# Kernel tuning notes

Measured on AMD Instinct MI355X. Metric: run time of the kernel, lower is better.

## Reference

```python
import jax, jax.numpy as jnp
import numpy as np

TEMPERATURE = 0.1
N, D = 4096, 1024


def setup_inputs() -> dict:
    key = jax.random.key(0)
    k1, k2 = jax.random.split(key)
    return {
        "embeddings1": jax.random.normal(k1, (N, D), dtype=jnp.float32),
        "embeddings2": jax.random.normal(k2, (N, D), dtype=jnp.float32),
    }


def reference(embeddings1, embeddings2):
    # L2-normalize rows (eps matches torch F.normalize default 1e-12)
    e1 = embeddings1 / jnp.maximum(jnp.linalg.norm(embeddings1, axis=1, keepdims=True), 1e-12)
    e2 = embeddings2 / jnp.maximum(jnp.linalg.norm(embeddings2, axis=1, keepdims=True), 1e-12)

    # [N, N] pairwise logits; one GEMM replaces the N^2 Python-loop dots
    logits = jnp.einsum("nd,md->nm", e1, e2) / TEMPERATURE
    expS = jnp.exp(logits)
    diag = jnp.diagonal(expS)

    # denominators EXCLUDE the diagonal term (as in the original loop slicing)
    row_denom = jnp.sum(expS, axis=1) - diag  # sum over j != i of exp(s_ij)
    col_denom = jnp.sum(expS, axis=0) - diag  # sum over i != j of exp(s_ij)

    log_diag = jnp.diagonal(logits)
    sim_12 = jnp.sum(log_diag - jnp.log(row_denom))
    sim_21 = jnp.sum(log_diag - jnp.log(col_denom))
    return (-sim_12, -sim_21)
```

## Files before the change

### kernel.cpp

```cpp
#include <hip/hip_runtime.h>
#include <hip/hip_bf16.h>
#include <stdint.h>

#define NN 4096
#define DD 1024
#define SCL (10.0f / 4096.0f)

typedef float f32x4 __attribute__((ext_vector_type(4)));
typedef long long i64;

__device__ __forceinline__ void gload_lds16(const void* g, void* l) {
  __builtin_amdgcn_global_load_lds(
      (const __attribute__((address_space(1))) void*)g,
      (__attribute__((address_space(3))) void*)l, 16, 0, 0);
}

__global__ __launch_bounds__(256) void nrm_kernel(
    const float* __restrict__ e1, const float* __restrict__ e2,
    uint32_t* __restrict__ e1q, uint32_t* __restrict__ e2q,
    float* __restrict__ log_diag, float* __restrict__ exp_diag,
    float* __restrict__ row_sum, float* __restrict__ col_sum)
{
  const int row  = blockIdx.x;
  const int tid  = threadIdx.x;
  const int lane = tid & 63;
  const int wave = tid >> 6;
  const int64_t base = (int64_t)row * DD;

  const float4 v1 = *reinterpret_cast<const float4*>(e1 + base + tid * 4);
  const float4 v2 = *reinterpret_cast<const float4*>(e2 + base + tid * 4);

  float ss1 = v1.x*v1.x + v1.y*v1.y + v1.z*v1.z + v1.w*v1.w;
  float ss2 = v2.x*v2.x + v2.y*v2.y + v2.z*v2.z + v2.w*v2.w;
  float d12 = v1.x*v2.x + v1.y*v2.y + v1.z*v2.z + v1.w*v2.w;

  #pragma unroll
  for (int off = 1; off < 64; off <<= 1) {
    ss1 += __shfl_xor(ss1, off);
    ss2 += __shfl_xor(ss2, off);
    d12 += __shfl_xor(d12, off);
  }

  __shared__ float red[3][4];
  if (lane == 0) { red[0][wave] = ss1; red[1][wave] = ss2; red[2][wave] = d12; }
  __syncthreads();
  ss1 = red[0][0] + red[0][1] + red[0][2] + red[0][3];
  ss2 = red[1][0] + red[1][1] + red[1][2] + red[1][3];
  d12 = red[2][0] + red[2][1] + red[2][2] + red[2][3];

  const float inv1 = 1.0f / fmaxf(sqrtf(ss1), 1e-12f);
  const float inv2 = 1.0f / fmaxf(sqrtf(ss2), 1e-12f);

  if (tid == 0) {
    const float ld = d12 * inv1 * inv2 * 10.0f;
    log_diag[row] = ld;
    exp_diag[row] = __expf(ld);
    row_sum[row] = 0.0f;
    col_sum[row] = 0.0f;
  }

  const float s1 = inv1 * 64.0f;
  const float s2 = inv2 * 64.0f;
  int u1 = __builtin_amdgcn_cvt_pk_fp8_f32(v1.x * s1, v1.y * s1, 0, false);
  u1     = __builtin_amdgcn_cvt_pk_fp8_f32(v1.z * s1, v1.w * s1, u1, true);
  int u2 = __builtin_amdgcn_cvt_pk_fp8_f32(v2.x * s2, v2.y * s2, 0, false);
  u2     = __builtin_amdgcn_cvt_pk_fp8_f32(v2.z * s2, v2.w * s2, u2, true);
  e1q[row * (DD / 4) + tid] = (uint32_t)u1;
  e2q[row * (DD / 4) + tid] = (uint32_t)u2;
}

__global__ __launch_bounds__(512, 4) void gemm_kernel(
    const uint8_t* __restrict__ A,
    const uint8_t* __restrict__ B,
    float* __restrict__ row_sum, float* __restrict__ col_sum)
{
  __shared__ __align__(16) uint8_t lds_a[2][256][64];
  __shared__ __align__(16) uint8_t lds_b[2][128][64];

  const int tid  = threadIdx.x;
  const int lane = tid & 63;
  const int wave = tid >> 6;
  const int wm = wave >> 1;
  const int wn = wave & 1;

  const int bid = blockIdx.x;
  const int xcd = bid & 7;
  const int k   = bid >> 3;
  const int brow = ((xcd >> 1) * 4 + (k >> 4)) * 256;
  const int bcol = ((xcd & 1) * 16 + (k & 15)) * 128;

  const int fr = lane & 15;
  const int fq = lane >> 4;
  const int y  = ((fr >> 1) & 3) << 1;
  const int o0 = ((fq ^ y) * 8);

  const int s_chunk = ((lane & 3) ^ ((lane >> 3) & 3)) * 16;
  const uint8_t* a_src0 = A + (int64_t)(brow + wave * 32 + (lane >> 2)) * DD + s_chunk;
  const uint8_t* a_src1 = a_src0 + 16 * DD;
  const uint8_t* b_src  = B + (int64_t)(bcol + wave * 16 + (lane >> 2)) * DD + s_chunk;

  f32x4 acc[4][4] = {};

#define STAGE(n, kc)                                          \
  gload_lds16(a_src0 + (kc), &lds_a[n][wave * 32][0]);        \
  gload_lds16(a_src1 + (kc), &lds_a[n][wave * 32 + 16][0]);   \
  gload_lds16(b_src  + (kc), &lds_b[n][wave * 16][0]);

#define TILE(c, PF, KC)                                                        \
  {                                                                            \
    asm volatile("s_waitcnt vmcnt(0)" ::: "memory");                           \
    __builtin_amdgcn_s_barrier();                                              \
    i64 a0[4], b0[4], a1[4], b1[4];                                            \
    _Pragma("unroll")                                                          \
    for (int i = 0; i < 4; ++i)                                                \
      a0[i] = *reinterpret_cast<const i64*>(&lds_a[c][wm*64 + i*16 + fr][o0]); \
    _Pragma("unroll")                                                          \
    for (int j = 0; j < 4; ++j)                                                \
      b0[j] = *reinterpret_cast<const i64*>(&lds_b[c][wn*64 + j*16 + fr][o0]); \
    _Pragma("unroll")                                                          \
    for (int i = 0; i < 4; ++i)                                                \
      a1[i] = *reinterpret_cast<const i64*>(                                   \
          &lds_a[c][wm*64 + i*16 + fr][o0 ^ 32]);                              \
    _Pragma("unroll")                                                          \
    for (int j = 0; j < 4; ++j)                                                \
      b1[j] = *reinterpret_cast<const i64*>(                                   \
          &lds_b[c][wn*64 + j*16 + fr][o0 ^ 32]);                              \
    if (PF) { STAGE((c) ^ 1, KC) }                                             \
    __builtin_amdgcn_s_setprio(1);                                             \
    _Pragma("unroll")                                                          \
    for (int i = 0; i < 4; ++i) {                                              \
      _Pragma("unroll")                                                        \
      for (int j = 0; j < 4; ++j)                                              \
        acc[i][j] = __builtin_amdgcn_mfma_f32_16x16x32_fp8_fp8(                \
            a0[i], b0[j], acc[i][j], 0, 0, 0);                                 \
    }                                                                          \
    _Pragma("unroll")                                                          \
    for (int i = 0; i < 4; ++i) {                                              \
      _Pragma("unroll")                                                        \
      for (int j = 0; j < 4; ++j)                                              \
        acc[i][j] = __builtin_amdgcn_mfma_f32_16x16x32_fp8_fp8(                \
            a1[i], b1[j], acc[i][j], 0, 0, 0);                                 \
    }                                                                          \
    __builtin_amdgcn_s_setprio(0);                                             \
  }

  STAGE(0, 0)

  #pragma unroll 2
  for (int t = 0; t < DD / 64; ++t) {
    TILE(t & 1, t < DD / 64 - 1, (t + 1) * 64)
  }
#undef TILE
#undef STAGE

  float rowp[4][4];
  float colp[4];
  #pragma unroll
  for (int mi = 0; mi < 4; ++mi)
    #pragma unroll
    for (int j = 0; j < 4; ++j) rowp[mi][j] = 0.0f;
  #pragma unroll
  for (int ni = 0; ni < 4; ++ni) colp[ni] = 0.0f;

  #pragma unroll
  for (int mi = 0; mi < 4; ++mi) {
    #pragma unroll
    for (int ni = 0; ni < 4; ++ni) {
      #pragma unroll
      for (int j = 0; j < 4; ++j) {
        const float v = __expf(acc[mi][ni][j] * SCL);
        rowp[mi][j] += v;
        colp[ni]    += v;
      }
    }
  }

  #pragma unroll
  for (int mi = 0; mi < 4; ++mi) {
    #pragma unroll
    for (int j = 0; j < 4; ++j) {
      float r = rowp[mi][j];
      r += __shfl_xor(r, 1);
      r += __shfl_xor(r, 2);
      r += __shfl_xor(r, 4);
      r += __shfl_xor(r, 8);
      if (fr == 0) {
        atomicAdd(&row_sum[brow + wm * 64 + mi * 16 + fq * 4 + j], r);
      }
    }
  }
  #pragma unroll
  for (int ni = 0; ni < 4; ++ni) {
    float cc = colp[ni];
    cc += __shfl_xor(cc, 16);
    cc += __shfl_xor(cc, 32);
    if (lane < 16) {
      atomicAdd(&col_sum[bcol + wn * 64 + ni * 16 + fr], cc);
    }
  }
}

__global__ __launch_bounds__(1024) void fin_kernel(
    const float* __restrict__ row_sum, const float* __restrict__ col_sum,
    const float* __restrict__ log_diag, const float* __restrict__ exp_diag,
    float* __restrict__ out)
{
  const int tid  = threadIdx.x;
  const int lane = tid & 63;
  const int wave = tid >> 6;
  const float* sums = (blockIdx.x == 0) ? row_sum : col_sum;
  float a = 0.0f;
  #pragma unroll
  for (int kk = 0; kk < NN / 1024; ++kk) {
    const int i = tid + kk * 1024;
    a += logf(sums[i] - exp_diag[i]) - log_diag[i];
  }
  #pragma unroll
  for (int off = 1; off < 64; off <<= 1) a += __shfl_xor(a, off);
  __shared__ float r0[16];
  if (lane == 0) r0[wave] = a;
  __syncthreads();
  if (tid == 0) {
    float s = 0.0f;
    #pragma unroll
    for (int w = 0; w < 16; ++w) s += r0[w];
    out[blockIdx.x] = s;
  }
}

extern "C" void kernel_launch(void* const* d_in, const int* in_sizes, int n_in,
                              void* d_out, int out_size, void* d_ws, size_t ws_size,
                              hipStream_t stream) {
  const float* e1 = (const float*)d_in[0];
  const float* e2 = (const float*)d_in[1];
  float* out = (float*)d_out;

  char* ws = (char*)d_ws;
  uint32_t* e1q = (uint32_t*)ws;
  uint32_t* e2q = (uint32_t*)(ws + (size_t)NN * DD);
  float* log_diag = (float*)(ws + (size_t)NN * DD * 2);
  float* exp_diag = log_diag + NN;
  float* row_sum  = exp_diag + NN;
  float* col_sum  = row_sum + NN;

  nrm_kernel<<<NN, 256, 0, stream>>>(e1, e2, e1q, e2q, log_diag, exp_diag,
                                     row_sum, col_sum);
  gemm_kernel<<<512, 512, 0, stream>>>((const uint8_t*)e1q, (const uint8_t*)e2q,
                                       row_sum, col_sum);
  fin_kernel<<<2, 1024, 0, stream>>>(row_sum, col_sum, log_diag, exp_diag, out);
}
```

Measured before the change: 50.05 us.

## Enlarge GEMM block tile to 256x256 with triple-buffered LDS pipeline

The fp8 GEMM block tile grows from 256x128 to 256x256, so each wave now computes 128x64 outputs and the grid shrinks to 256 blocks. The LDS staging moves from a double buffer to a triple buffer with a prefetch distance of two and a partial vmcnt wait. Global-to-LDS loads are split into four pieces and interleaved between MFMA groups. The aim is better operand reuse and more overlap of memory loads with MFMA work. In exchange it uses more accumulator registers and more LDS, cuts occupancy to one block per CU, and leaves fewer blocks to spread the work.

```diff
diff --git a/kernel.cpp b/kernel.cpp
--- a/kernel.cpp
+++ b/kernel.cpp
@@ -69,101 +69,137 @@
   e2q[row * (DD / 4) + tid] = (uint32_t)u2;
 }
 
-__global__ __launch_bounds__(512, 4) void gemm_kernel(
+__global__ __launch_bounds__(512, 2) void gemm_kernel(
     const uint8_t* __restrict__ A,
     const uint8_t* __restrict__ B,
     float* __restrict__ row_sum, float* __restrict__ col_sum)
 {
-  __shared__ __align__(16) uint8_t lds_a[2][256][64];
-  __shared__ __align__(16) uint8_t lds_b[2][128][64];
+  __shared__ __align__(16) uint8_t lds_a[3][256][64];
+  __shared__ __align__(16) uint8_t lds_b[3][256][64];
 
   const int tid  = threadIdx.x;
   const int lane = tid & 63;
   const int wave = tid >> 6;
-  const int wm = wave >> 1;
-  const int wn = wave & 1;
+  const int wm = wave >> 2;
+  const int wn = wave & 3;
 
   const int bid = blockIdx.x;
   const int xcd = bid & 7;
   const int k   = bid >> 3;
-  const int brow = ((xcd >> 1) * 4 + (k >> 4)) * 256;
-  const int bcol = ((xcd & 1) * 16 + (k & 15)) * 128;
-
-  const int fr = lane & 15;
-  const int fq = lane >> 4;
-  const int y  = ((fr >> 1) & 3) << 1;
-  const int o0 = ((fq ^ y) * 8);
+  const int brow = ((xcd >> 1) * 4 + (k >> 3)) * 256;
+  const int bcol = ((xcd & 1) * 8 + (k & 7)) * 256;
+
+  const int fr  = lane & 15;
+  const int fq  = lane >> 4;
+  const int fq1 = fq & 1;
+  const int fq2 = fq >> 1;
+  const int frx = (fr >> 1) & 3;
+  const int o0  = ((fq2 ^ frx) << 4) + (fq1 << 3);
+  const int o1  = o0 ^ 32;
 
   const int s_chunk = ((lane & 3) ^ ((lane >> 3) & 3)) * 16;
-  const uint8_t* a_src0 = A + (int64_t)(brow + wave * 32 + (lane >> 2)) * DD + s_chunk;
-  const uint8_t* a_src1 = a_src0 + 16 * DD;
-  const uint8_t* b_src  = B + (int64_t)(bcol + wave * 16 + (lane >> 2)) * DD + s_chunk;
-
-  f32x4 acc[4][4] = {};
-
-#define STAGE(n, kc)                                          \
-  gload_lds16(a_src0 + (kc), &lds_a[n][wave * 32][0]);        \
-  gload_lds16(a_src1 + (kc), &lds_a[n][wave * 32 + 16][0]);   \
-  gload_lds16(b_src  + (kc), &lds_b[n][wave * 16][0]);
-
-#define TILE(c, PF, KC)                                                        \
-  {                                                                            \
-    asm volatile("s_waitcnt vmcnt(0)" ::: "memory");                           \
-    __builtin_amdgcn_s_barrier();                                              \
-    i64 a0[4], b0[4], a1[4], b1[4];                                            \
-    _Pragma("unroll")                                                          \
-    for (int i = 0; i < 4; ++i)                                                \
-      a0[i] = *reinterpret_cast<const i64*>(&lds_a[c][wm*64 + i*16 + fr][o0]); \
-    _Pragma("unroll")                                                          \
-    for (int j = 0; j < 4; ++j)                                                \
-      b0[j] = *reinterpret_cast<const i64*>(&lds_b[c][wn*64 + j*16 + fr][o0]); \
-    _Pragma("unroll")                                                          \
-    for (int i = 0; i < 4; ++i)                                                \
-      a1[i] = *reinterpret_cast<const i64*>(                                   \
-          &lds_a[c][wm*64 + i*16 + fr][o0 ^ 32]);                              \
-    _Pragma("unroll")                                                          \
-    for (int j = 0; j < 4; ++j)                                                \
-      b1[j] = *reinterpret_cast<const i64*>(                                   \
-          &lds_b[c][wn*64 + j*16 + fr][o0 ^ 32]);                              \
-    if (PF) { STAGE((c) ^ 1, KC) }                                             \
-    __builtin_amdgcn_s_setprio(1);                                             \
-    _Pragma("unroll")                                                          \
-    for (int i = 0; i < 4; ++i) {                                              \
-      _Pragma("unroll")                                                        \
-      for (int j = 0; j < 4; ++j)                                              \
-        acc[i][j] = __builtin_amdgcn_mfma_f32_16x16x32_fp8_fp8(                \
-            a0[i], b0[j], acc[i][j], 0, 0, 0);                                 \
-    }                                                                          \
-    _Pragma("unroll")                                                          \
-    for (int i = 0; i < 4; ++i) {                                              \
-      _Pragma("unroll")                                                        \
-      for (int j = 0; j < 4; ++j)                                              \
-        acc[i][j] = __builtin_amdgcn_mfma_f32_16x16x32_fp8_fp8(                \
-            a1[i], b1[j], acc[i][j], 0, 0, 0);                                 \
-    }                                                                          \
-    __builtin_amdgcn_s_setprio(0);                                             \
-  }
-
-  STAGE(0, 0)
-
-  #pragma unroll 2
-  for (int t = 0; t < DD / 64; ++t) {
-    TILE(t & 1, t < DD / 64 - 1, (t + 1) * 64)
-  }
+  const int s_row   = wave * 16 + (lane >> 2);
+  const uint8_t* a_src0 = A + (int64_t)(brow + s_row) * DD + s_chunk;
+  const uint8_t* a_src1 = a_src0 + 128 * DD;
+  const uint8_t* b_src0 = B + (int64_t)(bcol + s_row) * DD + s_chunk;
+  const uint8_t* b_src1 = b_src0 + 128 * DD;
+
+  f32x4 acc[8][4] = {};
+
+#define ST_A0(s, kc) gload_lds16(a_src0 + (kc), &lds_a[s][wave * 16][0]);
+#define ST_A1(s, kc) gload_lds16(a_src1 + (kc), &lds_a[s][128 + wave * 16][0]);
+#define ST_B0(s, kc) gload_lds16(b_src0 + (kc), &lds_b[s][wave * 16][0]);
+#define ST_B1(s, kc) gload_lds16(b_src1 + (kc), &lds_b[s][128 + wave * 16][0]);
+
+#define LDA(S, m, O) \
+  (*reinterpret_cast<const i64*>(&lds_a[S][wm * 128 + (m) * 16 + fr][O]))
+#define LDB(S, n, O) \
+  (*reinterpret_cast<const i64*>(&lds_b[S][wn * 64 + (n) * 16 + fr][O]))
+
+#define MF(m, n, av, bv)                                           \
+  acc[m][n] = __builtin_amdgcn_mfma_f32_16x16x32_fp8_fp8(          \
+      av, bv, acc[m][n], 0, 0, 0);
+
+#define MF16(MB, A0, A1, A2, A3)                                   \
+  MF(MB + 0, 0, A0, b0) MF(MB + 0, 1, A0, b1)                      \
+  MF(MB + 0, 2, A0, b2) MF(MB + 0, 3, A0, b3)                      \
+  MF(MB + 1, 0, A1, b0) MF(MB + 1, 1, A1, b1)                      \
+  MF(MB + 1, 2, A1, b2) MF(MB + 1, 3, A1, b3)                      \
+  MF(MB + 2, 0, A2, b0) MF(MB + 2, 1, A2, b1)                      \
+  MF(MB + 2, 2, A2, b2) MF(MB + 2, 3, A2, b3)                      \
+  MF(MB + 3, 0, A3, b0) MF(MB + 3, 1, A3, b1)                      \
+  MF(MB + 3, 2, A3, b2) MF(MB + 3, 3, A3, b3)
+
+#define TILE(S, PF, KC)                                                      \
+  {                                                                          \
+    const int SP = ((S) + 2) % 3;                                            \
+    i64 b0, b1, b2, b3, a0, a1, a2, a3;                                      \
+                                                      \
+    b0 = LDB(S, 0, o0); b1 = LDB(S, 1, o0);                                  \
+    b2 = LDB(S, 2, o0); b3 = LDB(S, 3, o0);                                  \
+    a0 = LDA(S, 0, o0); a1 = LDA(S, 1, o0);                                  \
+    a2 = LDA(S, 2, o0); a3 = LDA(S, 3, o0);                                  \
+    if (PF) { ST_A0(SP, KC) }                                                \
+    __builtin_amdgcn_s_setprio(1);                                           \
+    MF16(0, a0, a1, a2, a3)                                                  \
+    __builtin_amdgcn_s_setprio(0);                                           \
+                                       \
+    a0 = LDA(S, 4, o0); a1 = LDA(S, 5, o0);                                  \
+    a2 = LDA(S, 6, o0); a3 = LDA(S, 7, o0);                                  \
+    if (PF) { ST_A1(SP, KC) }                                                \
+    __builtin_amdgcn_s_setprio(1);                                           \
+    MF16(4, a0, a1, a2, a3)                                                  \
+    __builtin_amdgcn_s_setprio(0);                                           \
+                                                      \
+    b0 = LDB(S, 0, o1); b1 = LDB(S, 1, o1);                                  \
+    b2 = LDB(S, 2, o1); b3 = LDB(S, 3, o1);                                  \
+    a0 = LDA(S, 0, o1); a1 = LDA(S, 1, o1);                                  \
+    a2 = LDA(S, 2, o1); a3 = LDA(S, 3, o1);                                  \
+    if (PF) { ST_B0(SP, KC) }                                                \
+    __builtin_amdgcn_s_setprio(1);                                           \
+    MF16(0, a0, a1, a2, a3)                                                  \
+    __builtin_amdgcn_s_setprio(0);                                           \
+                                       \
+    a0 = LDA(S, 4, o1); a1 = LDA(S, 5, o1);                                  \
+    a2 = LDA(S, 6, o1); a3 = LDA(S, 7, o1);                                  \
+    if (PF) { ST_B1(SP, KC) }                                                \
+    __builtin_amdgcn_s_setprio(1);                                           \
+    MF16(4, a0, a1, a2, a3)                                                  \
+    __builtin_amdgcn_s_setprio(0);                                           \
+  }
+
+  ST_A0(0, 0) ST_A1(0, 0) ST_B0(0, 0) ST_B1(0, 0)
+  ST_A0(1, 64) ST_A1(1, 64) ST_B0(1, 64) ST_B1(1, 64)
+
+  #pragma unroll 3
+  for (int t = 0; t < 15; ++t) {
+    asm volatile("s_waitcnt vmcnt(4)\n\ts_barrier" ::: "memory");
+    TILE(t % 3, (t <= 13), (t + 2) * 64)
+  }
+  asm volatile("s_waitcnt vmcnt(0)\n\ts_barrier" ::: "memory");
+  TILE(0, false, 0)
+
 #undef TILE
-#undef STAGE
-
-  float rowp[4][4];
+#undef MF16
+#undef MF
+#undef LDB
+#undef LDA
+#undef ST_B1
+#undef ST_B0
+#undef ST_A1
+#undef ST_A0
+
+  float rowp[8][4];
   float colp[4];
   #pragma unroll
-  for (int mi = 0; mi < 4; ++mi)
+  for (int mi = 0; mi < 8; ++mi)
     #pragma unroll
     for (int j = 0; j < 4; ++j) rowp[mi][j] = 0.0f;
   #pragma unroll
   for (int ni = 0; ni < 4; ++ni) colp[ni] = 0.0f;
 
   #pragma unroll
-  for (int mi = 0; mi < 4; ++mi) {
+  for (int mi = 0; mi < 8; ++mi) {
     #pragma unroll
     for (int ni = 0; ni < 4; ++ni) {
       #pragma unroll
@@ -176,7 +212,7 @@
   }
 
   #pragma unroll
-  for (int mi = 0; mi < 4; ++mi) {
+  for (int mi = 0; mi < 8; ++mi) {
     #pragma unroll
     for (int j = 0; j < 4; ++j) {
       float r = rowp[mi][j];
@@ -185,7 +221,7 @@
       r += __shfl_xor(r, 4);
       r += __shfl_xor(r, 8);
       if (fr == 0) {
-        atomicAdd(&row_sum[brow + wm * 64 + mi * 16 + fq * 4 + j], r);
+        atomicAdd(&row_sum[brow + wm * 128 + mi * 16 + fq * 4 + j], r);
       }
     }
   }
@@ -245,7 +281,7 @@
 
   nrm_kernel<<<NN, 256, 0, stream>>>(e1, e2, e1q, e2q, log_diag, exp_diag,
                                      row_sum, col_sum);
-  gemm_kernel<<<512, 512, 0, stream>>>((const uint8_t*)e1q, (const uint8_t*)e2q,
+  gemm_kernel<<<256, 512, 0, stream>>>((const uint8_t*)e1q, (const uint8_t*)e2q,
                                        row_sum, col_sum);
   fin_kernel<<<2, 1024, 0, stream>>>(row_sum, col_sum, log_diag, exp_diag, out);
 }
```

Result: slower. 52.29 us (+4.5%).
